# Kernel tuning notes

Hardware: AMD Instinct MI355X
Metric: run time of the kernel (lower is better)

## Reference

```python
import jax, jax.numpy as jnp
import numpy as np

SIZE = (160, 192, 160)  # matches init_kwargs `size`


def _make_grid(size):
    # torch: meshgrid(arange(s) for s, indexing='ij'), stack last dim, flip last dim
    vecs = [jnp.arange(s, dtype=jnp.float32) for s in size]
    g = jnp.stack(jnp.meshgrid(*vecs, indexing='ij'), axis=-1)
    g = g[..., ::-1]  # last-dim order becomes (x, y, z) = (W, H, D) indices
    return g[None]    # [1, D, H, W, 3]


def _grid_sample_3d(src, locs):
    """Trilinear grid_sample, align_corners=True, padding_mode='zeros'.
    src: [B, C, D, H, W]; locs: [B, D, H, W, 3] in [-1,1], last dim (x,y,z)."""
    B, C, D, H, W = src.shape
    dims_m1 = jnp.array([W - 1, H - 1, D - 1], jnp.float32)
    px = (locs + 1.0) * 0.5 * dims_m1  # unnormalize (align_corners=True)
    x, y, z = px[..., 0], px[..., 1], px[..., 2]
    x0 = jnp.floor(x); y0 = jnp.floor(y); z0 = jnp.floor(z)
    fx, fy, fz = x - x0, y - y0, z - z0
    x0i = x0.astype(jnp.int32); y0i = y0.astype(jnp.int32); z0i = z0.astype(jnp.int32)

    def gather(src_b, iz, iy, ix):  # src_b: [C,D,H,W]; idx: [D,H,W]
        return src_b[:, iz, iy, ix]  # [C,D,H,W]

    out = jnp.zeros(src.shape, src.dtype)
    for dz in (0, 1):
        for dy in (0, 1):
            for dx in (0, 1):
                ix, iy, iz = x0i + dx, y0i + dy, z0i + dz
                valid = (ix >= 0) & (ix < W) & (iy >= 0) & (iy < H) & (iz >= 0) & (iz < D)
                w = ((fx if dx else 1.0 - fx)
                     * (fy if dy else 1.0 - fy)
                     * (fz if dz else 1.0 - fz))
                w = jnp.where(valid, w, 0.0)  # zero padding for OOB
                icx = jnp.clip(ix, 0, W - 1)
                icy = jnp.clip(iy, 0, H - 1)
                icz = jnp.clip(iz, 0, D - 1)
                v = jax.vmap(gather)(src, icz, icy, icx)  # [B,C,D,H,W]
                out = out + w[:, None] * v
    return out


def setup_inputs() -> dict:
    key = jax.random.key(0)
    k1, k2 = jax.random.split(key)
    B, C = 2, 2
    D, H, W = SIZE
    src = jax.random.normal(k1, (B, C, D, H, W), dtype=jnp.float32)
    flow = jax.random.normal(k2, (B, 3, D, H, W), dtype=jnp.float32)
    return {"src": src, "flow": flow}


def reference(src, flow):
    # order='image': no flip of flow channels
    flow = jnp.moveaxis(flow, 1, -1)                      # [B,D,H,W,3]
    grid = _make_grid(SIZE)                                # [1,D,H,W,3]
    s = jnp.array(SIZE, jnp.float32)[::-1] - 1.0           # [W-1,H-1,D-1]
    new_locs = 2.0 * ((grid + flow) / s - 0.5)             # normalized [-1,1]
    return _grid_sample_3d(src, new_locs)
```

## Files before the change

### kernel.cpp

```cpp
#include <hip/hip_runtime.h>

#define DD 160
#define HH 192
#define WW 160
#define SP (DD * HH * WW)
#define NB 2
#define NC 2

#define TX 32
#define TY 8
#define TZ 8
#define RXW 40
#define RYH 15
#define RZD 15
#define REGC (RZD * RYH * RXW)
#define NCHUNK (REGC / 4)
#define NITER 5

#define NTX 5
#define NTY 24
#define NTZ 20
#define NTILES (NTX * NTY * NTZ * NB)
#define PER_XCD (NTILES / 8)

typedef float v2f __attribute__((ext_vector_type(2)));
typedef float v4f __attribute__((ext_vector_type(4)));

__device__ __forceinline__ v4f ld4_nt(const float* p) {
    return __builtin_nontemporal_load(reinterpret_cast<const v4f*>(p));
}
__device__ __forceinline__ void st4_nt(float* p, v4f v) {
    __builtin_nontemporal_store(v, reinterpret_cast<v4f*>(p));
}
__device__ __forceinline__ v2f ld2g(const float* p) {
    return *reinterpret_cast<const v2f*>(p);
}
__device__ __forceinline__ v2f s2(float f) { v2f v = {f, f}; return v; }

__device__ __forceinline__ void sample_global(
    const float* __restrict__ s0, const float* __restrict__ s1,
    int x, int y, int z, float dx, float dy, float dz,
    float& a0, float& a1)
{
    float sx = (float)x + dx, sy = (float)y + dy, sz = (float)z + dz;
    float xf = floorf(sx), yf = floorf(sy), zf = floorf(sz);
    float fx = sx - xf, fy = sy - yf, fz = sz - zf;
    int x0 = (int)xf, y0 = (int)yf, z0 = (int)zf;
    int x1 = x0 + 1, y1 = y0 + 1, z1 = z0 + 1;

    float wx0 = (x0 >= 0 && x0 < WW) ? (1.0f - fx) : 0.0f;
    float wx1 = (x1 >= 0 && x1 < WW) ? fx : 0.0f;
    float wy0 = (y0 >= 0 && y0 < HH) ? (1.0f - fy) : 0.0f;
    float wy1 = (y1 >= 0 && y1 < HH) ? fy : 0.0f;
    float wz0 = (z0 >= 0 && z0 < DD) ? (1.0f - fz) : 0.0f;
    float wz1 = (z1 >= 0 && z1 < DD) ? fz : 0.0f;

    int p  = min(max(x0, 0), WW - 2);
    int i0 = min(max(x0, 0), WW - 1) - p;
    int i1 = min(max(x1, 0), WW - 1) - p;
    int cy0 = min(max(y0, 0), HH - 1), cy1 = min(max(y1, 0), HH - 1);
    int cz0 = min(max(z0, 0), DD - 1), cz1 = min(max(z1, 0), DD - 1);

    int o00 = (cz0 * HH + cy0) * WW + p;
    int o01 = (cz0 * HH + cy1) * WW + p;
    int o10 = (cz1 * HH + cy0) * WW + p;
    int o11 = (cz1 * HH + cy1) * WW + p;

    float w00 = wz0 * wy0, w01 = wz0 * wy1, w10 = wz1 * wy0, w11 = wz1 * wy1;

    v2f c0_00 = ld2g(s0 + o00); v2f c1_00 = ld2g(s1 + o00);
    v2f c0_01 = ld2g(s0 + o01); v2f c1_01 = ld2g(s1 + o01);
    v2f c0_10 = ld2g(s0 + o10); v2f c1_10 = ld2g(s1 + o10);
    v2f c0_11 = ld2g(s0 + o11); v2f c1_11 = ld2g(s1 + o11);

    #define PICK(v, i) ((i) ? (v).y : (v).x)
    float r0, r1;
    r0  = w00 * (wx0 * PICK(c0_00, i0) + wx1 * PICK(c0_00, i1));
    r1  = w00 * (wx0 * PICK(c1_00, i0) + wx1 * PICK(c1_00, i1));
    r0 += w01 * (wx0 * PICK(c0_01, i0) + wx1 * PICK(c0_01, i1));
    r1 += w01 * (wx0 * PICK(c1_01, i0) + wx1 * PICK(c1_01, i1));
    r0 += w10 * (wx0 * PICK(c0_10, i0) + wx1 * PICK(c0_10, i1));
    r1 += w10 * (wx0 * PICK(c1_10, i0) + wx1 * PICK(c1_10, i1));
    r0 += w11 * (wx0 * PICK(c0_11, i0) + wx1 * PICK(c0_11, i1));
    r1 += w11 * (wx0 * PICK(c1_11, i0) + wx1 * PICK(c1_11, i1));
    #undef PICK
    a0 = r0; a1 = r1;
}

__global__ __launch_bounds__(512, 4) void st_warp_kernel(
    const float* __restrict__ src,
    const float* __restrict__ flow,
    float* __restrict__ out)
{
    __shared__ float sbuf[2 * REGC];

    int u   = blockIdx.x;
    int tl  = (u & 7) * PER_XCD + (u >> 3);
    int tx  = tl % NTX;  int t2 = tl / NTX;
    int ty  = t2 % NTY;  int t3 = t2 / NTY;
    int tz  = t3 % NTZ;  int b  = t3 / NTZ;
    int X0 = tx * TX, Y0 = ty * TY, Z0 = tz * TZ;
    int tid = threadIdx.x;

    const float* sb = src + b * NC * SP;

    v4f va[NITER], vb[NITER];
    int  ad[NITER];
    #pragma unroll
    for (int i = 0; i < NITER; ++i) {
        int c = tid + i * 512;
        if (i < NITER - 1 || c < NCHUNK) {
            int lz  = c / 150;  int r2 = c - lz * 150;
            int ly  = r2 / 10;  int lxc = r2 - ly * 10;
            int mz = min(max(Z0 - 3 + lz, 0), DD - 1);
            int my = min(max(Y0 - 3 + ly, 0), HH - 1);
            int mx = X0 - 4 + lxc * 4;
            const float* p = sb + (mz * HH + my) * WW;
            v4f A, B;
            if (mx >= 0 && mx <= WW - 4) {
                A = *reinterpret_cast<const v4f*>(p + mx);
                B = *reinterpret_cast<const v4f*>(p + SP + mx);
            } else {
                int m0 = min(max(mx,     0), WW - 1);
                int m1 = min(max(mx + 1, 0), WW - 1);
                int m2 = min(max(mx + 2, 0), WW - 1);
                int m3 = min(max(mx + 3, 0), WW - 1);
                A.x = p[m0]; A.y = p[m1]; A.z = p[m2]; A.w = p[m3];
                B.x = p[SP + m0]; B.y = p[SP + m1]; B.z = p[SP + m2]; B.w = p[SP + m3];
            }
            va[i] = A; vb[i] = B;
            ad[i] = 2 * ((lz * RYH + ly) * RXW + lxc * 4);
        } else {
            ad[i] = -1;
        }
    }

    int rr = tid >> 3;
    int xi = (tid & 7) << 2;
    int yl = rr & 7, zl = rr >> 3;
    int y = Y0 + yl, z = Z0 + zl, x = X0 + xi;
    int fo = b * 3 * SP + (z * HH + y) * WW + x;
    v4f dxv = ld4_nt(flow + fo);
    v4f dyv = ld4_nt(flow + fo + SP);
    v4f dzv = ld4_nt(flow + fo + 2 * SP);

    #pragma unroll
    for (int i = 0; i < NITER; ++i) {
        if (ad[i] >= 0) {
            v4f w0 = {va[i].x, vb[i].x, va[i].y, vb[i].y};
            v4f w1 = {va[i].z, vb[i].z, va[i].w, vb[i].w};
            *reinterpret_cast<v4f*>(&sbuf[ad[i]])     = w0;
            *reinterpret_cast<v4f*>(&sbuf[ad[i] + 4]) = w1;
        }
    }
    __syncthreads();

    const int rx0 = X0 - 4, ry0 = Y0 - 3, rz0 = Z0 - 3;
    float a0[4], a1[4];
    #pragma unroll
    for (int j = 0; j < 4; ++j) {
        float dx = dxv[j], dy = dyv[j], dz = dzv[j];
        bool inH = (dx >= -4.0f) & (dx < 4.0f) &
                   (dy >= -3.0f) & (dy < 4.0f) &
                   (dz >= -3.0f) & (dz < 4.0f);
        if (inH) {
            float lx = (float)(xi + j + 4) + dx;
            float ly = (float)(yl + 3) + dy;
            float lz = (float)(zl + 3) + dz;
            float xf = floorf(lx), yf = floorf(ly), zf = floorf(lz);
            float fx = lx - xf, fy = ly - yf, fz = lz - zf;
            int ix = (int)xf, iy = (int)yf, iz = (int)zf;

            int vx0 = ix + rx0, vy0 = iy + ry0, vz0 = iz + rz0;
            float wx0 = (vx0 >= 0  && vx0 < WW)     ? (1.0f - fx) : 0.0f;
            float wx1 = (vx0 >= -1 && vx0 < WW - 1) ? fx          : 0.0f;
            float wy0 = (vy0 >= 0  && vy0 < HH)     ? (1.0f - fy) : 0.0f;
            float wy1 = (vy0 >= -1 && vy0 < HH - 1) ? fy          : 0.0f;
            float wz0 = (vz0 >= 0  && vz0 < DD)     ? (1.0f - fz) : 0.0f;
            float wz1 = (vz0 >= -1 && vz0 < DD - 1) ? fz          : 0.0f;

            const float* pB = sbuf + 2 * ((iz * RYH + iy) * RXW + ix);
            v2f A00 = *(const v2f*)(pB);
            v2f B00 = *(const v2f*)(pB + 2);
            v2f A01 = *(const v2f*)(pB + 2 * RXW);
            v2f B01 = *(const v2f*)(pB + 2 * RXW + 2);
            const float* pC = pB + 2 * RYH * RXW;
            v2f A10 = *(const v2f*)(pC);
            v2f B10 = *(const v2f*)(pC + 2);
            v2f A11 = *(const v2f*)(pC + 2 * RXW);
            v2f B11 = *(const v2f*)(pC + 2 * RXW + 2);

            v2f c00 = s2(wx0) * A00 + s2(wx1) * B00;
            v2f c01 = s2(wx0) * A01 + s2(wx1) * B01;
            v2f c10 = s2(wx0) * A10 + s2(wx1) * B10;
            v2f c11 = s2(wx0) * A11 + s2(wx1) * B11;
            v2f m0  = s2(wy0) * c00 + s2(wy1) * c01;
            v2f m1  = s2(wy0) * c10 + s2(wy1) * c11;
            v2f r   = s2(wz0) * m0  + s2(wz1) * m1;
            a0[j] = r.x; a1[j] = r.y;
        } else {
            sample_global(sb, sb + SP, x + j, y, z, dx, dy, dz, a0[j], a1[j]);
        }
    }

    int oo = b * NC * SP + (z * HH + y) * WW + x;
    v4f o0 = {a0[0], a0[1], a0[2], a0[3]};
    v4f o1 = {a1[0], a1[1], a1[2], a1[3]};
    st4_nt(out + oo, o0);
    st4_nt(out + oo + SP, o1);
}

extern "C" void kernel_launch(void* const* d_in, const int* in_sizes, int n_in,
                              void* d_out, int out_size, void* d_ws, size_t ws_size,
                              hipStream_t stream) {
    const float* src  = (const float*)d_in[0];
    const float* flow = (const float*)d_in[1];
    float* out = (float*)d_out;

    st_warp_kernel<<<NTILES, 512, 0, stream>>>(src, flow, out);
}
```

Measured before the change: 267.1 us.

## Stage channels sequentially through a halved LDS buffer to raise occupancy

The LDS halo tile now holds a single channel instead of two interleaved channels, halving shared memory per block. Each channel is loaded, synchronised and sampled in turn, and the launch bounds ask for 8 blocks per CU instead of 4. This aims to raise occupancy and latency hiding, but it adds two extra barriers, serialises the second channel's global load behind the first channel's compute, and turns vectorised paired LDS reads into scalar ones. Samples that take the global fallback path still handle both channels in the first pass.

New measurement: 350.5 us. 1.31x slower.

```diff
diff --git a/kernel.cpp b/kernel.cpp
--- a/kernel.cpp
+++ b/kernel.cpp
@@ -35,7 +35,6 @@
 __device__ __forceinline__ v2f ld2g(const float* p) {
     return *reinterpret_cast<const v2f*>(p);
 }
-__device__ __forceinline__ v2f s2(float f) { v2f v = {f, f}; return v; }
 
 __device__ __forceinline__ void sample_global(
     const float* __restrict__ s0, const float* __restrict__ s1,
@@ -87,25 +86,10 @@
     a0 = r0; a1 = r1;
 }
 
-__global__ __launch_bounds__(512, 4) void st_warp_kernel(
-    const float* __restrict__ src,
-    const float* __restrict__ flow,
-    float* __restrict__ out)
-{
-    __shared__ float sbuf[2 * REGC];
-
-    int u   = blockIdx.x;
-    int tl  = (u & 7) * PER_XCD + (u >> 3);
-    int tx  = tl % NTX;  int t2 = tl / NTX;
-    int ty  = t2 % NTY;  int t3 = t2 / NTY;
-    int tz  = t3 % NTZ;  int b  = t3 / NTZ;
-    int X0 = tx * TX, Y0 = ty * TY, Z0 = tz * TZ;
-    int tid = threadIdx.x;
-
-    const float* sb = src + b * NC * SP;
-
-    v4f va[NITER], vb[NITER];
-    int  ad[NITER];
+__device__ __forceinline__ void stage_issue(
+    const float* __restrict__ cb, int X0, int Y0, int Z0, int tid,
+    v4f* v, int* ad)
+{
     #pragma unroll
     for (int i = 0; i < NITER; ++i) {
         int c = tid + i * 512;
@@ -115,25 +99,87 @@
             int mz = min(max(Z0 - 3 + lz, 0), DD - 1);
             int my = min(max(Y0 - 3 + ly, 0), HH - 1);
             int mx = X0 - 4 + lxc * 4;
-            const float* p = sb + (mz * HH + my) * WW;
-            v4f A, B;
+            const float* p = cb + (mz * HH + my) * WW;
+            v4f A;
             if (mx >= 0 && mx <= WW - 4) {
                 A = *reinterpret_cast<const v4f*>(p + mx);
-                B = *reinterpret_cast<const v4f*>(p + SP + mx);
             } else {
                 int m0 = min(max(mx,     0), WW - 1);
                 int m1 = min(max(mx + 1, 0), WW - 1);
                 int m2 = min(max(mx + 2, 0), WW - 1);
                 int m3 = min(max(mx + 3, 0), WW - 1);
                 A.x = p[m0]; A.y = p[m1]; A.z = p[m2]; A.w = p[m3];
-                B.x = p[SP + m0]; B.y = p[SP + m1]; B.z = p[SP + m2]; B.w = p[SP + m3];
             }
-            va[i] = A; vb[i] = B;
-            ad[i] = 2 * ((lz * RYH + ly) * RXW + lxc * 4);
+            v[i] = A;
+            ad[i] = (lz * RYH + ly) * RXW + lxc * 4;
         } else {
             ad[i] = -1;
         }
     }
+}
+
+__device__ __forceinline__ void stage_write(float* sbuf, const v4f* v, const int* ad)
+{
+    #pragma unroll
+    for (int i = 0; i < NITER; ++i) {
+        if (ad[i] >= 0) {
+            *reinterpret_cast<v4f*>(&sbuf[ad[i]]) = v[i];
+        }
+    }
+}
+
+__device__ __forceinline__ float sample_lds(
+    const float* __restrict__ sbuf,
+    float lx, float ly, float lz, int rx0, int ry0, int rz0)
+{
+    float xf = floorf(lx), yf = floorf(ly), zf = floorf(lz);
+    float fx = lx - xf, fy = ly - yf, fz = lz - zf;
+    int ix = (int)xf, iy = (int)yf, iz = (int)zf;
+
+    int vx0 = ix + rx0, vy0 = iy + ry0, vz0 = iz + rz0;
+    float wx0 = (vx0 >= 0  && vx0 < WW)     ? (1.0f - fx) : 0.0f;
+    float wx1 = (vx0 >= -1 && vx0 < WW - 1) ? fx          : 0.0f;
+    float wy0 = (vy0 >= 0  && vy0 < HH)     ? (1.0f - fy) : 0.0f;
+    float wy1 = (vy0 >= -1 && vy0 < HH - 1) ? fy          : 0.0f;
+    float wz0 = (vz0 >= 0  && vz0 < DD)     ? (1.0f - fz) : 0.0f;
+    float wz1 = (vz0 >= -1 && vz0 < DD - 1) ? fz          : 0.0f;
+
+    const float* pB = sbuf + (iz * RYH + iy) * RXW + ix;
+    float A00 = pB[0],        B00 = pB[1];
+    float A01 = pB[RXW],      B01 = pB[RXW + 1];
+    const float* pC = pB + RYH * RXW;
+    float A10 = pC[0],        B10 = pC[1];
+    float A11 = pC[RXW],      B11 = pC[RXW + 1];
+
+    float c00 = wx0 * A00 + wx1 * B00;
+    float c01 = wx0 * A01 + wx1 * B01;
+    float c10 = wx0 * A10 + wx1 * B10;
+    float c11 = wx0 * A11 + wx1 * B11;
+    float m0  = wy0 * c00 + wy1 * c01;
+    float m1  = wy0 * c10 + wy1 * c11;
+    return wz0 * m0 + wz1 * m1;
+}
+
+__global__ __launch_bounds__(512, 8) void st_warp_kernel(
+    const float* __restrict__ src,
+    const float* __restrict__ flow,
+    float* __restrict__ out)
+{
+    __shared__ float sbuf[REGC];
+
+    int u   = blockIdx.x;
+    int tl  = (u & 7) * PER_XCD + (u >> 3);
+    int tx  = tl % NTX;  int t2 = tl / NTX;
+    int ty  = t2 % NTY;  int t3 = t2 / NTY;
+    int tz  = t3 % NTZ;  int b  = t3 / NTZ;
+    int X0 = tx * TX, Y0 = ty * TY, Z0 = tz * TZ;
+    int tid = threadIdx.x;
+
+    const float* sb = src + b * NC * SP;
+
+    v4f vs[NITER];
+    int  ad[NITER];
+    stage_issue(sb, X0, Y0, Z0, tid, vs, ad);
 
     int rr = tid >> 3;
     int xi = (tid & 7) << 2;
@@ -144,15 +190,7 @@
     v4f dyv = ld4_nt(flow + fo + SP);
     v4f dzv = ld4_nt(flow + fo + 2 * SP);
 
-    #pragma unroll
-    for (int i = 0; i < NITER; ++i) {
-        if (ad[i] >= 0) {
-            v4f w0 = {va[i].x, vb[i].x, va[i].y, vb[i].y};
-            v4f w1 = {va[i].z, vb[i].z, va[i].w, vb[i].w};
-            *reinterpret_cast<v4f*>(&sbuf[ad[i]])     = w0;
-            *reinterpret_cast<v4f*>(&sbuf[ad[i] + 4]) = w1;
-        }
-    }
+    stage_write(sbuf, vs, ad);
     __syncthreads();
 
     const int rx0 = X0 - 4, ry0 = Y0 - 3, rz0 = Z0 - 3;
@@ -167,39 +205,28 @@
             float lx = (float)(xi + j + 4) + dx;
             float ly = (float)(yl + 3) + dy;
             float lz = (float)(zl + 3) + dz;
-            float xf = floorf(lx), yf = floorf(ly), zf = floorf(lz);
-            float fx = lx - xf, fy = ly - yf, fz = lz - zf;
-            int ix = (int)xf, iy = (int)yf, iz = (int)zf;
-
-            int vx0 = ix + rx0, vy0 = iy + ry0, vz0 = iz + rz0;
-            float wx0 = (vx0 >= 0  && vx0 < WW)     ? (1.0f - fx) : 0.0f;
-            float wx1 = (vx0 >= -1 && vx0 < WW - 1) ? fx          : 0.0f;
-            float wy0 = (vy0 >= 0  && vy0 < HH)     ? (1.0f - fy) : 0.0f;
-            float wy1 = (vy0 >= -1 && vy0 < HH - 1) ? fy          : 0.0f;
-            float wz0 = (vz0 >= 0  && vz0 < DD)     ? (1.0f - fz) : 0.0f;
-            float wz1 = (vz0 >= -1 && vz0 < DD - 1) ? fz          : 0.0f;
-
-            const float* pB = sbuf + 2 * ((iz * RYH + iy) * RXW + ix);
-            v2f A00 = *(const v2f*)(pB);
-            v2f B00 = *(const v2f*)(pB + 2);
-            v2f A01 = *(const v2f*)(pB + 2 * RXW);
-            v2f B01 = *(const v2f*)(pB + 2 * RXW + 2);
-            const float* pC = pB + 2 * RYH * RXW;
-            v2f A10 = *(const v2f*)(pC);
-            v2f B10 = *(const v2f*)(pC + 2);
-            v2f A11 = *(const v2f*)(pC + 2 * RXW);
-            v2f B11 = *(const v2f*)(pC + 2 * RXW + 2);
-
-            v2f c00 = s2(wx0) * A00 + s2(wx1) * B00;
-            v2f c01 = s2(wx0) * A01 + s2(wx1) * B01;
-            v2f c10 = s2(wx0) * A10 + s2(wx1) * B10;
-            v2f c11 = s2(wx0) * A11 + s2(wx1) * B11;
-            v2f m0  = s2(wy0) * c00 + s2(wy1) * c01;
-            v2f m1  = s2(wy0) * c10 + s2(wy1) * c11;
-            v2f r   = s2(wz0) * m0  + s2(wz1) * m1;
-            a0[j] = r.x; a1[j] = r.y;
+            a0[j] = sample_lds(sbuf, lx, ly, lz, rx0, ry0, rz0);
         } else {
             sample_global(sb, sb + SP, x + j, y, z, dx, dy, dz, a0[j], a1[j]);
+        }
+    }
+    __syncthreads();
+
+    stage_issue(sb + SP, X0, Y0, Z0, tid, vs, ad);
+    stage_write(sbuf, vs, ad);
+    __syncthreads();
+
+    #pragma unroll
+    for (int j = 0; j < 4; ++j) {
+        float dx = dxv[j], dy = dyv[j], dz = dzv[j];
+        bool inH = (dx >= -4.0f) & (dx < 4.0f) &
+                   (dy >= -3.0f) & (dy < 4.0f) &
+                   (dz >= -3.0f) & (dz < 4.0f);
+        if (inH) {
+            float lx = (float)(xi + j + 4) + dx;
+            float ly = (float)(yl + 3) + dy;
+            float lz = (float)(zl + 3) + dz;
+            a1[j] = sample_lds(sbuf, lx, ly, lz, rx0, ry0, rz0);
         }
     }
 
```
